# Performance work log

Hardware: AMD Instinct MI355X
Metric: run time of the kernel (lower is better)

Reference implementation:

```python
import jax, jax.numpy as jnp
import numpy as np

# dims per init_kwargs / input_specs
N, F_IN, H, C, L = 50000, 128, 128, 40, 4
E = 800000
ALPHA = 0.1   # args.beta -> self.alpha (initial-residual strength)
LAMDA = 0.5   # identity-mapping decay


def setup_inputs() -> dict:
    key = jax.random.key(0)
    ks = jax.random.split(key, 6)
    x = jax.random.normal(ks[0], (N, F_IN), jnp.float32)
    edge_index = jax.random.randint(ks[1], (2, E), 0, N, dtype=jnp.int32)
    s = 1.0 / np.sqrt(H)
    W_in = jax.random.uniform(ks[2], (F_IN, H), jnp.float32, -s, s)
    b_in = jnp.zeros((H,), jnp.float32)
    W_layers = jax.random.uniform(ks[3], (L, H, H), jnp.float32, -s, s)
    W_out = jax.random.uniform(ks[4], (H, C), jnp.float32, -s, s)
    b_out = jnp.zeros((C,), jnp.float32)
    return dict(x=x, edge_index=edge_index, W_in=W_in, b_in=b_in,
                W_layers=W_layers, W_out=W_out, b_out=b_out)


def _gcn_norm(edge_index, n):
    """Symmetric GCN normalization with added self-loops (gcn_norm)."""
    loops = jnp.arange(n, dtype=edge_index.dtype)
    row = jnp.concatenate([edge_index[0], loops])  # destination
    col = jnp.concatenate([edge_index[1], loops])  # source
    deg = jax.ops.segment_sum(jnp.ones(row.shape, jnp.float32), row, num_segments=n)
    dinv = jnp.where(deg > 0, jax.lax.rsqrt(jnp.maximum(deg, 1e-12)), 0.0)
    return row, col, dinv[row] * dinv[col]  # per-edge norm coefficient


def reference(x, edge_index, W_in, b_in, W_layers, W_out, b_out):
    n = x.shape[0]
    row, col, norm = _gcn_norm(edge_index, n)
    # input linear + relu (dropout is identity in eval / p=0)
    h = jax.nn.relu(x @ W_in + b_in)
    h0 = h  # _hidden[0], the initial residual
    # beta_i = log(lamda/(i+1) + 1)
    betas = jnp.log(LAMDA / jnp.arange(1, L + 1, dtype=jnp.float32) + 1.0)

    def layer(h, wb):
        W, beta = wb
        # sparse graph conv: gather-source, scale, scatter-add to dest  [E,H] msgs
        agg = jax.ops.segment_sum(h[col] * norm[:, None], row, num_segments=n)
        support = (1.0 - ALPHA) * agg + ALPHA * h0
        out = beta * (support @ W) + (1.0 - beta) * support  # ((1-b)I + bW)
        return jax.nn.relu(out), None

    h, _ = jax.lax.scan(layer, h, (W_layers, betas))
    return h @ W_out + b_out
```

## Files before the change

kernel.cpp:

```cpp
#include <hip/hip_runtime.h>
#include <hip/hip_bf16.h>
#include <hip/hip_fp16.h>
#include <math.h>

typedef short short8 __attribute__((ext_vector_type(8)));
typedef _Float16 half8 __attribute__((ext_vector_type(8)));
typedef float f32x4  __attribute__((ext_vector_type(4)));

__device__ __forceinline__ unsigned short f2h(float f) {
    return __half_as_ushort(__float2half(f));
}
__device__ __forceinline__ float h2f(unsigned short u) {
    return __half2float(__ushort_as_half(u));
}


__global__ void k_count(const int* __restrict__ dst, int* __restrict__ cnt,
                        unsigned short* __restrict__ rank, int E) {
    int t = blockIdx.x * 256 + threadIdx.x;
    int e = t * 4;
    if (e + 3 < E) {
        int4 d = *(const int4*)&dst[e];
        unsigned r0 = atomicAdd(&cnt[d.x], 1);
        unsigned r1 = atomicAdd(&cnt[d.y], 1);
        unsigned r2 = atomicAdd(&cnt[d.z], 1);
        unsigned r3 = atomicAdd(&cnt[d.w], 1);
        *(ushort4*)&rank[e] = make_ushort4((unsigned short)r0, (unsigned short)r1,
                                           (unsigned short)r2, (unsigned short)r3);
    } else {
        for (; e < E; ++e)
            rank[e] = (unsigned short)atomicAdd(&cnt[dst[e]], 1);
    }
}

__global__ void k_scan_part(const int* __restrict__ cnt, int* __restrict__ offs,
                            int* __restrict__ parts, float* __restrict__ dinv, int n) {
    __shared__ int s[256];
    int i = blockIdx.x * 256 + threadIdx.x;
    int v = (i < n) ? cnt[i] : 0;
    s[threadIdx.x] = v;
    __syncthreads();
    #pragma unroll
    for (int d = 1; d < 256; d <<= 1) {
        int t = (threadIdx.x >= d) ? s[threadIdx.x - d] : 0;
        __syncthreads();
        s[threadIdx.x] += t;
        __syncthreads();
    }
    if (i < n) {
        offs[i] = s[threadIdx.x] - v;
        dinv[i] = rsqrtf((float)v + 1.0f);
    }
    if (threadIdx.x == 255) parts[blockIdx.x] = s[255];
}

__global__ void k_scan_tops(int* __restrict__ parts, int np) {
    __shared__ int s[256];
    int tid = threadIdx.x;
    int v = (tid < np) ? parts[tid] : 0;
    s[tid] = v;
    __syncthreads();
    #pragma unroll
    for (int d = 1; d < 256; d <<= 1) {
        int t = (tid >= d) ? s[tid - d] : 0;
        __syncthreads();
        s[tid] += t;
        __syncthreads();
    }
    if (tid < np) parts[tid] = s[tid] - v;
}

__global__ void k_scan_add(int* __restrict__ offs, const int* __restrict__ parts,
                           int n, int e_total) {
    int i = blockIdx.x * 256 + threadIdx.x;
    if (i < n) offs[i] += parts[blockIdx.x];
    if (blockIdx.x == 0 && threadIdx.x == 0) offs[n] = e_total;
}

__global__ void k_scatter(const int* __restrict__ dst, const int* __restrict__ src,
                          const unsigned short* __restrict__ rank,
                          const int* __restrict__ offs,
                          const float* __restrict__ dinv,
                          unsigned* __restrict__ csr, int E) {
    int t = blockIdx.x * 256 + threadIdx.x;
    int e = t * 4;
    if (e + 3 < E) {
        int4 d = *(const int4*)&dst[e];
        int4 s = *(const int4*)&src[e];
        ushort4 r = *(const ushort4*)&rank[e];
        float dd0 = dinv[d.x], dd1 = dinv[d.y], dd2 = dinv[d.z], dd3 = dinv[d.w];
        float ds0 = dinv[s.x], ds1 = dinv[s.y], ds2 = dinv[s.z], ds3 = dinv[s.w];
        int o0 = offs[d.x], o1 = offs[d.y], o2 = offs[d.z], o3 = offs[d.w];
        csr[o0 + r.x] = ((unsigned)f2h(0.9f * dd0 * ds0) << 16) | (unsigned)s.x;
        csr[o1 + r.y] = ((unsigned)f2h(0.9f * dd1 * ds1) << 16) | (unsigned)s.y;
        csr[o2 + r.z] = ((unsigned)f2h(0.9f * dd2 * ds2) << 16) | (unsigned)s.z;
        csr[o3 + r.w] = ((unsigned)f2h(0.9f * dd3 * ds3) << 16) | (unsigned)s.w;
    } else {
        for (; e < E; ++e) {
            int d = dst[e], s = src[e];
            float w = 0.9f * dinv[d] * dinv[s];
            csr[offs[d] + (int)rank[e]] = ((unsigned)f2h(w) << 16) | (unsigned)s;
        }
    }
}


__global__ void k_wprep(const float* __restrict__ Wl, const float* __restrict__ Win,
                        const float* __restrict__ Wout,
                        unsigned short* __restrict__ wt,
                        unsigned short* __restrict__ wint,
                        unsigned short* __restrict__ wot, int C,
                        uint4* __restrict__ cntz, int n16) {
    int m = blockIdx.x;
    if (m < 4) {
        for (int i = threadIdx.x; i < 16384; i += 256) {
            int n = i >> 7, k = i & 127;
            wt[m * 16384 + n * 128 + k] = f2h(Wl[m * 16384 + k * 128 + n]);
        }
    } else if (m == 4) {
        for (int i = threadIdx.x; i < 16384; i += 256) {
            int n = i >> 7, k = i & 127;
            wint[n * 128 + k] = f2h(Win[k * 128 + n]);
        }
    } else if (m == 5) {
        for (int i = threadIdx.x; i < 48 * 128; i += 256) {
            int n = i >> 7, k = i & 127;
            wot[n * 128 + k] = (n < C) ? f2h(Wout[k * C + n]) : (unsigned short)0;
        }
    } else {
        int i = (m - 6) * 256 + threadIdx.x;
        if (i < n16) cntz[i] = make_uint4(0u, 0u, 0u, 0u);
    }
}


__global__ __launch_bounds__(256)
void k_spmm(const int* __restrict__ offs, const unsigned* __restrict__ csr,
            const unsigned short* __restrict__ hb,
            const unsigned short* __restrict__ h0b,
            const float* __restrict__ dinv,
            unsigned short* __restrict__ supb, int n, int E) {
    int node = blockIdx.x * 8 + (threadIdx.x >> 5);
    if (node >= n) return;
    int l32 = threadIdx.x & 31;
    float di = dinv[node];
    float ws = 0.9f * di * di;
    uint2 sv = *(const uint2*)&hb [((size_t)node << 7) + (l32 << 2)];
    uint2 rv = *(const uint2*)&h0b[((size_t)node << 7) + (l32 << 2)];
    float ax = ws * h2f((unsigned short)(sv.x & 0xffffu)) + 0.1f * h2f((unsigned short)(rv.x & 0xffffu));
    float ay = ws * h2f((unsigned short)(sv.x >> 16))     + 0.1f * h2f((unsigned short)(rv.x >> 16));
    float az = ws * h2f((unsigned short)(sv.y & 0xffffu)) + 0.1f * h2f((unsigned short)(rv.y & 0xffffu));
    float aw = ws * h2f((unsigned short)(sv.y >> 16))     + 0.1f * h2f((unsigned short)(rv.y >> 16));
    int e = offs[node], end = offs[node + 1];
    while (e < end) {
        int nb = end - e;
        if (nb > 32) nb = 32;
        unsigned ce = csr[min(e + l32, E - 1)];
        int i = 0;
        for (; i + 16 <= nb; i += 16) {
            uint2 g[16]; float wv[16];
            #pragma unroll
            for (int j = 0; j < 16; ++j) {
                unsigned u = __shfl(ce, i + j, 32);
                wv[j] = h2f((unsigned short)(u >> 16));
                g[j] = *(const uint2*)&hb[((size_t)(u & 0xffffu) << 7) + (l32 << 2)];
            }
            #pragma unroll
            for (int j = 0; j < 16; ++j) {
                ax += wv[j] * h2f((unsigned short)(g[j].x & 0xffffu));
                ay += wv[j] * h2f((unsigned short)(g[j].x >> 16));
                az += wv[j] * h2f((unsigned short)(g[j].y & 0xffffu));
                aw += wv[j] * h2f((unsigned short)(g[j].y >> 16));
            }
        }
        for (; i + 8 <= nb; i += 8) {
            uint2 g[8]; float wv[8];
            #pragma unroll
            for (int j = 0; j < 8; ++j) {
                unsigned u = __shfl(ce, i + j, 32);
                wv[j] = h2f((unsigned short)(u >> 16));
                g[j] = *(const uint2*)&hb[((size_t)(u & 0xffffu) << 7) + (l32 << 2)];
            }
            #pragma unroll
            for (int j = 0; j < 8; ++j) {
                ax += wv[j] * h2f((unsigned short)(g[j].x & 0xffffu));
                ay += wv[j] * h2f((unsigned short)(g[j].x >> 16));
                az += wv[j] * h2f((unsigned short)(g[j].y & 0xffffu));
                aw += wv[j] * h2f((unsigned short)(g[j].y >> 16));
            }
        }
        for (; i + 4 <= nb; i += 4) {
            uint2 g[4]; float wv[4];
            #pragma unroll
            for (int j = 0; j < 4; ++j) {
                unsigned u = __shfl(ce, i + j, 32);
                wv[j] = h2f((unsigned short)(u >> 16));
                g[j] = *(const uint2*)&hb[((size_t)(u & 0xffffu) << 7) + (l32 << 2)];
            }
            #pragma unroll
            for (int j = 0; j < 4; ++j) {
                ax += wv[j] * h2f((unsigned short)(g[j].x & 0xffffu));
                ay += wv[j] * h2f((unsigned short)(g[j].x >> 16));
                az += wv[j] * h2f((unsigned short)(g[j].y & 0xffffu));
                aw += wv[j] * h2f((unsigned short)(g[j].y >> 16));
            }
        }
        for (; i + 2 <= nb; i += 2) {
            uint2 g[2]; float wv[2];
            #pragma unroll
            for (int j = 0; j < 2; ++j) {
                unsigned u = __shfl(ce, i + j, 32);
                wv[j] = h2f((unsigned short)(u >> 16));
                g[j] = *(const uint2*)&hb[((size_t)(u & 0xffffu) << 7) + (l32 << 2)];
            }
            #pragma unroll
            for (int j = 0; j < 2; ++j) {
                ax += wv[j] * h2f((unsigned short)(g[j].x & 0xffffu));
                ay += wv[j] * h2f((unsigned short)(g[j].x >> 16));
                az += wv[j] * h2f((unsigned short)(g[j].y & 0xffffu));
                aw += wv[j] * h2f((unsigned short)(g[j].y >> 16));
            }
        }
        for (; i < nb; ++i) {
            unsigned u = __shfl(ce, i, 32);
            float w = h2f((unsigned short)(u >> 16));
            uint2 g = *(const uint2*)&hb[((size_t)(u & 0xffffu) << 7) + (l32 << 2)];
            ax += w * h2f((unsigned short)(g.x & 0xffffu));
            ay += w * h2f((unsigned short)(g.x >> 16));
            az += w * h2f((unsigned short)(g.y & 0xffffu));
            aw += w * h2f((unsigned short)(g.y >> 16));
        }
        e += nb;
    }
    uint2 o;
    o.x = (unsigned)f2h(ax) | ((unsigned)f2h(ay) << 16);
    o.y = (unsigned)f2h(az) | ((unsigned)f2h(aw) << 16);
    *(uint2*)&supb[((size_t)node << 7) + (l32 << 2)] = o;
}


__global__ __launch_bounds__(256)
void gemm_in(const float* __restrict__ inA,
             const unsigned short* __restrict__ Bh,
             const float* __restrict__ bias,
             unsigned short* __restrict__ hb,
             unsigned short* __restrict__ h0b, int M) {
    extern __shared__ char lds[];
    char* Ah = lds;
    char* Wh = Ah + 16384;

    const int tid  = threadIdx.x;
    const int row0 = blockIdx.x * 64;

    for (int c = tid; c < 1024; c += 256) {
        int row = c >> 4, k8 = c & 15;
        int grow = row0 + row;
        short8 hv = {0,0,0,0,0,0,0,0};
        if (grow < M) {
            const float* s = &inA[(size_t)grow * 128 + k8 * 8];
            float4 f0 = *(const float4*)s;
            float4 f1 = *(const float4*)(s + 4);
            float ff[8] = {f0.x, f0.y, f0.z, f0.w, f1.x, f1.y, f1.z, f1.w};
            #pragma unroll
            for (int j = 0; j < 8; ++j) hv[j] = (short)f2h(ff[j]);
        }
        *(short8*)(Ah + row * 256 + ((k8 ^ (row & 7)) << 4)) = hv;
    }
    for (int c = tid; c < 2048; c += 256) {
        int n = c >> 4, k8 = c & 15;
        *(short8*)(Wh + n * 256 + ((k8 ^ (n & 7)) << 4)) = *(const short8*)&Bh[n * 128 + k8 * 8];
    }
    __syncthreads();

    const int lane = tid & 63;
    const int w    = tid >> 6;
    const int lr   = lane & 15;
    const int lg   = lane >> 4;

    f32x4 acc[4][2];
    #pragma unroll
    for (int m = 0; m < 4; ++m)
        #pragma unroll
        for (int n2 = 0; n2 < 2; ++n2) acc[m][n2] = (f32x4){0.f, 0.f, 0.f, 0.f};

    #pragma unroll
    for (int kk = 0; kk < 4; ++kk) {
        int k8 = kk * 4 + lg;
        half8 a[4], b[2];
        #pragma unroll
        for (int m = 0; m < 4; ++m) {
            int row = m * 16 + lr;
            a[m] = *(const half8*)(Ah + row * 256 + ((k8 ^ (row & 7)) << 4));
        }
        #pragma unroll
        for (int n2 = 0; n2 < 2; ++n2) {
            int n = (w * 2 + n2) * 16 + lr;
            b[n2] = *(const half8*)(Wh + n * 256 + ((k8 ^ (n & 7)) << 4));
        }
        #pragma unroll
        for (int m = 0; m < 4; ++m)
            #pragma unroll
            for (int n2 = 0; n2 < 2; ++n2)
                acc[m][n2] = __builtin_amdgcn_mfma_f32_16x16x32_f16(a[m], b[n2], acc[m][n2], 0, 0, 0);
    }

    #pragma unroll
    for (int m = 0; m < 4; ++m) {
        #pragma unroll
        for (int n2 = 0; n2 < 2; ++n2) {
            int col = (w * 2 + n2) * 16 + lr;
            #pragma unroll
            for (int r = 0; r < 4; ++r) {
                int row = row0 + m * 16 + lg * 4 + r;
                if (row < M) {
                    float o = fmaxf(acc[m][n2][r] + bias[col], 0.f);
                    unsigned short ob = f2h(o);
                    hb [(size_t)row * 128 + col] = ob;
                    h0b[(size_t)row * 128 + col] = ob;
                }
            }
        }
    }
}


__global__ __launch_bounds__(512)
void gemm_layer(const unsigned short* __restrict__ supb,
                const unsigned short* __restrict__ Bh,
                float beta, float gamma,
                unsigned short* __restrict__ outh, int M) {
    extern __shared__ char lds[];
    char* Ah = lds;
    char* Wh = Ah + 32768;

    const int tid  = threadIdx.x;
    const int row0 = blockIdx.x * 128;

    for (int c = tid; c < 2048; c += 512) {
        int row = c >> 4, k8 = c & 15;
        int grow = row0 + row;
        short8 hv = {0,0,0,0,0,0,0,0};
        if (grow < M) hv = *(const short8*)&supb[(size_t)grow * 128 + k8 * 8];
        *(short8*)(Ah + row * 256 + ((k8 ^ (row & 7)) << 4)) = hv;
    }
    for (int c = tid; c < 2048; c += 512) {
        int n = c >> 4, k8 = c & 15;
        *(short8*)(Wh + n * 256 + ((k8 ^ (n & 7)) << 4)) = *(const short8*)&Bh[n * 128 + k8 * 8];
    }
    __syncthreads();

    const int lane = tid & 63;
    const int w    = tid >> 6;
    const int wr   = w >> 1;
    const int wc   = w & 1;
    const int lr   = lane & 15;
    const int lg   = lane >> 4;

    f32x4 acc[2][4];
    #pragma unroll
    for (int m = 0; m < 2; ++m)
        #pragma unroll
        for (int n2 = 0; n2 < 4; ++n2) acc[m][n2] = (f32x4){0.f, 0.f, 0.f, 0.f};

    #pragma unroll
    for (int kk = 0; kk < 4; ++kk) {
        int k8 = kk * 4 + lg;
        half8 a[2], b[4];
        #pragma unroll
        for (int m = 0; m < 2; ++m) {
            int row = wr * 32 + m * 16 + lr;
            a[m] = *(const half8*)(Ah + row * 256 + ((k8 ^ (row & 7)) << 4));
        }
        #pragma unroll
        for (int n2 = 0; n2 < 4; ++n2) {
            int n = wc * 64 + n2 * 16 + lr;
            b[n2] = *(const half8*)(Wh + n * 256 + ((k8 ^ (n & 7)) << 4));
        }
        #pragma unroll
        for (int m = 0; m < 2; ++m)
            #pragma unroll
            for (int n2 = 0; n2 < 4; ++n2)
                acc[m][n2] = __builtin_amdgcn_mfma_f32_16x16x32_f16(a[m], b[n2], acc[m][n2], 0, 0, 0);
    }

    #pragma unroll
    for (int m = 0; m < 2; ++m) {
        #pragma unroll
        for (int n2 = 0; n2 < 4; ++n2) {
            int col = wc * 64 + n2 * 16 + lr;
            int k8c = col >> 3;
            int ebc = (col & 7) * 2;
            #pragma unroll
            for (int r = 0; r < 4; ++r) {
                int rl  = wr * 32 + m * 16 + lg * 4 + r;
                int row = row0 + rl;
                if (row < M) {
                    unsigned short rb = *(const unsigned short*)
                        (Ah + rl * 256 + ((k8c ^ (rl & 7)) << 4) + ebc);
                    float o = beta * acc[m][n2][r] + gamma * h2f(rb);
                    o = fmaxf(o, 0.f);
                    outh[(size_t)row * 128 + col] = f2h(o);
                }
            }
        }
    }
}


__global__ __launch_bounds__(256)
void k_out(const unsigned short* __restrict__ hb,
           const unsigned short* __restrict__ Wot,
           const float* __restrict__ bias,
           float* __restrict__ out, int M, int C) {
    extern __shared__ char lds[];
    char* Ah = lds;
    char* Wh = Ah + 16384;

    const int tid  = threadIdx.x;
    const int row0 = blockIdx.x * 64;

    for (int c = tid; c < 1024; c += 256) {
        int row = c >> 4, k8 = c & 15;
        int grow = row0 + row;
        short8 hv = {0,0,0,0,0,0,0,0};
        if (grow < M) hv = *(const short8*)&hb[(size_t)grow * 128 + k8 * 8];
        *(short8*)(Ah + row * 256 + ((k8 ^ (row & 7)) << 4)) = hv;
    }
    for (int c = tid; c < 768; c += 256) {
        int n = c >> 4, k8 = c & 15;
        *(short8*)(Wh + n * 256 + ((k8 ^ (n & 7)) << 4)) = *(const short8*)&Wot[n * 128 + k8 * 8];
    }
    __syncthreads();

    const int lane = tid & 63;
    const int w    = tid >> 6;
    const int lr   = lane & 15;
    const int lg   = lane >> 4;

    f32x4 acc[3];
    #pragma unroll
    for (int n2 = 0; n2 < 3; ++n2) acc[n2] = (f32x4){0.f, 0.f, 0.f, 0.f};

    #pragma unroll
    for (int kk = 0; kk < 4; ++kk) {
        int k8 = kk * 4 + lg;
        int row = w * 16 + lr;
        half8 a = *(const half8*)(Ah + row * 256 + ((k8 ^ (row & 7)) << 4));
        #pragma unroll
        for (int n2 = 0; n2 < 3; ++n2) {
            int n = n2 * 16 + lr;
            half8 b = *(const half8*)(Wh + n * 256 + ((k8 ^ (n & 7)) << 4));
            acc[n2] = __builtin_amdgcn_mfma_f32_16x16x32_f16(a, b, acc[n2], 0, 0, 0);
        }
    }

    #pragma unroll
    for (int n2 = 0; n2 < 3; ++n2) {
        int col = n2 * 16 + lr;
        if (col < C) {
            float bb = bias[col];
            #pragma unroll
            for (int r = 0; r < 4; ++r) {
                int row = row0 + w * 16 + lg * 4 + r;
                if (row < M) out[(size_t)row * C + col] = acc[n2][r] + bb;
            }
        }
    }
}


extern "C" void kernel_launch(void* const* d_in, const int* in_sizes, int n_in,
                              void* d_out, int out_size, void* d_ws, size_t ws_size,
                              hipStream_t stream) {
    const float* x        = (const float*)d_in[0];
    const int*   ei       = (const int*)d_in[1];
    const float* W_in     = (const float*)d_in[2];
    const float* b_in     = (const float*)d_in[3];
    const float* W_layers = (const float*)d_in[4];
    const float* W_out    = (const float*)d_in[5];
    const float* b_out    = (const float*)d_in[6];
    float* out = (float*)d_out;

    const int H = 128;
    const int N = in_sizes[0] / H;
    const int E = in_sizes[1] / 2;
    const int L = in_sizes[4] / (H * H);
    const int C = in_sizes[5] / H;

    char* p = (char*)d_ws;
    auto alloc = [&](size_t bytes) {
        char* r = p;
        p += (bytes + 255) & ~(size_t)255;
        return r;
    };
    int*      cnt   = (int*)alloc((size_t)N * 4);
    int*      offs  = (int*)alloc((size_t)(N + 1) * 4);
    int*      parts = (int*)alloc(256 * 4);
    unsigned* csr   = (unsigned*)alloc((size_t)E * 4);
    unsigned short* rank = (unsigned short*)alloc((size_t)E * 2);
    float*    dinv  = (float*)alloc((size_t)N * 4);
    unsigned short* hb   = (unsigned short*)alloc((size_t)N * H * 2);
    unsigned short* h0b  = (unsigned short*)alloc((size_t)N * H * 2);
    unsigned short* supb = (unsigned short*)alloc((size_t)N * H * 2);
    unsigned short* wt   = (unsigned short*)alloc((size_t)L * H * H * 2);
    unsigned short* wint = (unsigned short*)alloc((size_t)H * H * 2);
    unsigned short* wot  = (unsigned short*)alloc((size_t)48 * H * 2);
    (void)ws_size;

    const int* ei0 = ei;
    const int* ei1 = ei + E;

    const int nblkN  = (N + 255) / 256;
    const int nblkE4 = ((E + 3) / 4 + 255) / 256;
    const int n16    = (N + 3) / 4;
    const int zblk   = (n16 + 255) / 256;

    k_wprep<<<6 + zblk, 256, 0, stream>>>(W_layers, W_in, W_out, wt, wint, wot, C,
                                          (uint4*)cnt, n16);

    k_count<<<nblkE4, 256, 0, stream>>>(ei0, cnt, rank, E);
    k_scan_part<<<nblkN, 256, 0, stream>>>(cnt, offs, parts, dinv, N);
    k_scan_tops<<<1, 256, 0, stream>>>(parts, nblkN);
    k_scan_add<<<nblkN, 256, 0, stream>>>(offs, parts, N, E);
    k_scatter<<<nblkE4, 256, 0, stream>>>(ei0, ei1, rank, offs, dinv, csr, E);

    gemm_in<<<(N + 63) / 64, 256, 48 * 1024, stream>>>(x, wint, b_in, hb, h0b, N);

    for (int l = 0; l < L; ++l) {
        float beta = logf(0.5f / (float)(l + 1) + 1.0f);
        k_spmm<<<(N + 7) / 8, 256, 0, stream>>>(offs, csr, hb, h0b, dinv, supb, N, E);
        gemm_layer<<<(N + 127) / 128, 512, 64 * 1024, stream>>>(
            supb, wt + (size_t)l * H * H, beta, 1.0f - beta, hb, N);
    }

    k_out<<<(N + 63) / 64, 256, 28 * 1024, stream>>>(hb, wot, b_out, out, N, C);
}
```

Baseline: 281.5 us.

## Widen CSR build to 8 edges/thread, skip h0 load on first layer, use nontemporal memory ops

k_count and k_scatter now handle 8 edges per thread instead of 4, so fewer threads each issue more independent atomics and gathers. k_spmm is templated so that on the first layer, where h equals h0, the residual is folded into the self-loop weight and the separate h0 read is dropped. CSR entry loads, h0 loads and support stores use nontemporal hints so streaming data does not crowd out the gathered h rows in cache. The changes are small and local, and their net effect on a memory-bound gather kernel depends on cache behaviour.

```diff
diff --git a/kernel.cpp b/kernel.cpp
--- a/kernel.cpp
+++ b/kernel.cpp
@@ -18,15 +18,22 @@
 __global__ void k_count(const int* __restrict__ dst, int* __restrict__ cnt,
                         unsigned short* __restrict__ rank, int E) {
     int t = blockIdx.x * 256 + threadIdx.x;
-    int e = t * 4;
-    if (e + 3 < E) {
-        int4 d = *(const int4*)&dst[e];
-        unsigned r0 = atomicAdd(&cnt[d.x], 1);
-        unsigned r1 = atomicAdd(&cnt[d.y], 1);
-        unsigned r2 = atomicAdd(&cnt[d.z], 1);
-        unsigned r3 = atomicAdd(&cnt[d.w], 1);
-        *(ushort4*)&rank[e] = make_ushort4((unsigned short)r0, (unsigned short)r1,
-                                           (unsigned short)r2, (unsigned short)r3);
+    int e = t * 8;
+    if (e + 7 < E) {
+        int4 d0 = *(const int4*)&dst[e];
+        int4 d1 = *(const int4*)&dst[e + 4];
+        unsigned r0 = atomicAdd(&cnt[d0.x], 1);
+        unsigned r1 = atomicAdd(&cnt[d0.y], 1);
+        unsigned r2 = atomicAdd(&cnt[d0.z], 1);
+        unsigned r3 = atomicAdd(&cnt[d0.w], 1);
+        unsigned r4 = atomicAdd(&cnt[d1.x], 1);
+        unsigned r5 = atomicAdd(&cnt[d1.y], 1);
+        unsigned r6 = atomicAdd(&cnt[d1.z], 1);
+        unsigned r7 = atomicAdd(&cnt[d1.w], 1);
+        *(ushort4*)&rank[e]     = make_ushort4((unsigned short)r0, (unsigned short)r1,
+                                               (unsigned short)r2, (unsigned short)r3);
+        *(ushort4*)&rank[e + 4] = make_ushort4((unsigned short)r4, (unsigned short)r5,
+                                               (unsigned short)r6, (unsigned short)r7);
     } else {
         for (; e < E; ++e)
             rank[e] = (unsigned short)atomicAdd(&cnt[dst[e]], 1);
@@ -83,18 +90,23 @@
                           const float* __restrict__ dinv,
                           unsigned* __restrict__ csr, int E) {
     int t = blockIdx.x * 256 + threadIdx.x;
-    int e = t * 4;
-    if (e + 3 < E) {
-        int4 d = *(const int4*)&dst[e];
-        int4 s = *(const int4*)&src[e];
-        ushort4 r = *(const ushort4*)&rank[e];
-        float dd0 = dinv[d.x], dd1 = dinv[d.y], dd2 = dinv[d.z], dd3 = dinv[d.w];
-        float ds0 = dinv[s.x], ds1 = dinv[s.y], ds2 = dinv[s.z], ds3 = dinv[s.w];
-        int o0 = offs[d.x], o1 = offs[d.y], o2 = offs[d.z], o3 = offs[d.w];
-        csr[o0 + r.x] = ((unsigned)f2h(0.9f * dd0 * ds0) << 16) | (unsigned)s.x;
-        csr[o1 + r.y] = ((unsigned)f2h(0.9f * dd1 * ds1) << 16) | (unsigned)s.y;
-        csr[o2 + r.z] = ((unsigned)f2h(0.9f * dd2 * ds2) << 16) | (unsigned)s.z;
-        csr[o3 + r.w] = ((unsigned)f2h(0.9f * dd3 * ds3) << 16) | (unsigned)s.w;
+    int e = t * 8;
+    if (e + 7 < E) {
+        int d[8], s[8];
+        *(int4*)&d[0] = *(const int4*)&dst[e];
+        *(int4*)&d[4] = *(const int4*)&dst[e + 4];
+        *(int4*)&s[0] = *(const int4*)&src[e];
+        *(int4*)&s[4] = *(const int4*)&src[e + 4];
+        ushort4 ra = *(const ushort4*)&rank[e];
+        ushort4 rb = *(const ushort4*)&rank[e + 4];
+        unsigned short r[8] = {ra.x, ra.y, ra.z, ra.w, rb.x, rb.y, rb.z, rb.w};
+        float dd[8], ds[8];
+        int   oo[8];
+        #pragma unroll
+        for (int j = 0; j < 8; ++j) { dd[j] = dinv[d[j]]; ds[j] = dinv[s[j]]; oo[j] = offs[d[j]]; }
+        #pragma unroll
+        for (int j = 0; j < 8; ++j)
+            csr[oo[j] + (int)r[j]] = ((unsigned)f2h(0.9f * dd[j] * ds[j]) << 16) | (unsigned)s[j];
     } else {
         for (; e < E; ++e) {
             int d = dst[e], s = src[e];
@@ -134,6 +146,7 @@
 }
 
 
+template<int FIRST>
 __global__ __launch_bounds__(256)
 void k_spmm(const int* __restrict__ offs, const unsigned* __restrict__ csr,
             const unsigned short* __restrict__ hb,
@@ -144,18 +157,26 @@
     if (node >= n) return;
     int l32 = threadIdx.x & 31;
     float di = dinv[node];
-    float ws = 0.9f * di * di;
-    uint2 sv = *(const uint2*)&hb [((size_t)node << 7) + (l32 << 2)];
-    uint2 rv = *(const uint2*)&h0b[((size_t)node << 7) + (l32 << 2)];
-    float ax = ws * h2f((unsigned short)(sv.x & 0xffffu)) + 0.1f * h2f((unsigned short)(rv.x & 0xffffu));
-    float ay = ws * h2f((unsigned short)(sv.x >> 16))     + 0.1f * h2f((unsigned short)(rv.x >> 16));
-    float az = ws * h2f((unsigned short)(sv.y & 0xffffu)) + 0.1f * h2f((unsigned short)(rv.y & 0xffffu));
-    float aw = ws * h2f((unsigned short)(sv.y >> 16))     + 0.1f * h2f((unsigned short)(rv.y >> 16));
+    float ws = 0.9f * di * di + (FIRST ? 0.1f : 0.0f);
+    uint2 sv = *(const uint2*)&hb[((size_t)node << 7) + (l32 << 2)];
+    float ax = ws * h2f((unsigned short)(sv.x & 0xffffu));
+    float ay = ws * h2f((unsigned short)(sv.x >> 16));
+    float az = ws * h2f((unsigned short)(sv.y & 0xffffu));
+    float aw = ws * h2f((unsigned short)(sv.y >> 16));
+    if (!FIRST) {
+        const unsigned* rp = (const unsigned*)&h0b[((size_t)node << 7) + (l32 << 2)];
+        unsigned rx = __builtin_nontemporal_load(rp);
+        unsigned ry = __builtin_nontemporal_load(rp + 1);
+        ax += 0.1f * h2f((unsigned short)(rx & 0xffffu));
+        ay += 0.1f * h2f((unsigned short)(rx >> 16));
+        az += 0.1f * h2f((unsigned short)(ry & 0xffffu));
+        aw += 0.1f * h2f((unsigned short)(ry >> 16));
+    }
     int e = offs[node], end = offs[node + 1];
     while (e < end) {
         int nb = end - e;
         if (nb > 32) nb = 32;
-        unsigned ce = csr[min(e + l32, E - 1)];
+        unsigned ce = __builtin_nontemporal_load(&csr[min(e + l32, E - 1)]);
         int i = 0;
         for (; i + 16 <= nb; i += 16) {
             uint2 g[16]; float wv[16];
@@ -232,10 +253,9 @@
         }
         e += nb;
     }
-    uint2 o;
-    o.x = (unsigned)f2h(ax) | ((unsigned)f2h(ay) << 16);
-    o.y = (unsigned)f2h(az) | ((unsigned)f2h(aw) << 16);
-    *(uint2*)&supb[((size_t)node << 7) + (l32 << 2)] = o;
+    unsigned* op = (unsigned*)&supb[((size_t)node << 7) + (l32 << 2)];
+    __builtin_nontemporal_store((unsigned)f2h(ax) | ((unsigned)f2h(ay) << 16), op);
+    __builtin_nontemporal_store((unsigned)f2h(az) | ((unsigned)f2h(aw) << 16), op + 1);
 }
 
 
@@ -511,24 +531,27 @@
     const int* ei1 = ei + E;
 
     const int nblkN  = (N + 255) / 256;
-    const int nblkE4 = ((E + 3) / 4 + 255) / 256;
+    const int nblkE8 = ((E + 7) / 8 + 255) / 256;
     const int n16    = (N + 3) / 4;
     const int zblk   = (n16 + 255) / 256;
 
     k_wprep<<<6 + zblk, 256, 0, stream>>>(W_layers, W_in, W_out, wt, wint, wot, C,
                                           (uint4*)cnt, n16);
 
-    k_count<<<nblkE4, 256, 0, stream>>>(ei0, cnt, rank, E);
+    k_count<<<nblkE8, 256, 0, stream>>>(ei0, cnt, rank, E);
     k_scan_part<<<nblkN, 256, 0, stream>>>(cnt, offs, parts, dinv, N);
     k_scan_tops<<<1, 256, 0, stream>>>(parts, nblkN);
     k_scan_add<<<nblkN, 256, 0, stream>>>(offs, parts, N, E);
-    k_scatter<<<nblkE4, 256, 0, stream>>>(ei0, ei1, rank, offs, dinv, csr, E);
+    k_scatter<<<nblkE8, 256, 0, stream>>>(ei0, ei1, rank, offs, dinv, csr, E);
 
     gemm_in<<<(N + 63) / 64, 256, 48 * 1024, stream>>>(x, wint, b_in, hb, h0b, N);
 
     for (int l = 0; l < L; ++l) {
         float beta = logf(0.5f / (float)(l + 1) + 1.0f);
-        k_spmm<<<(N + 7) / 8, 256, 0, stream>>>(offs, csr, hb, h0b, dinv, supb, N, E);
+        if (l == 0)
+            k_spmm<1><<<(N + 7) / 8, 256, 0, stream>>>(offs, csr, hb, h0b, dinv, supb, N, E);
+        else
+            k_spmm<0><<<(N + 7) / 8, 256, 0, stream>>>(offs, csr, hb, h0b, dinv, supb, N, E);
         gemm_layer<<<(N + 127) / 128, 512, 64 * 1024, stream>>>(
             supb, wt + (size_t)l * H * H, beta, 1.0f - beta, hb, N);
     }
```

Result: no change. 283.8 us (+0.8%).
